# Optimization experiments

Measured on AMD Instinct MI355X. Metric: run time of the kernel, lower is better.

Reference implementation:

```python
import jax, jax.numpy as jnp
import numpy as np

N_NODES = 100000
N_EDGES = 1250000
NUM_RELS = 8
D_IN, D_HID, D_OUT = 64, 64, 32


def setup_inputs() -> dict:
    key = jax.random.key(0)
    ks = jax.random.split(key, 10)
    x = jax.random.normal(ks[0], (N_NODES, D_IN), dtype=jnp.float32)
    src = jax.random.randint(ks[1], (N_EDGES,), 0, N_NODES, dtype=jnp.int32)
    dst = jax.random.randint(ks[2], (N_EDGES,), 0, N_NODES, dtype=jnp.int32)
    edge_type = jax.random.randint(ks[3], (N_EDGES,), 0, NUM_RELS, dtype=jnp.int32)
    s1 = 1.0 / np.sqrt(D_IN)
    s2 = 1.0 / np.sqrt(D_HID)
    W1 = jax.random.uniform(ks[4], (NUM_RELS, D_IN, D_HID), jnp.float32, -s1, s1)
    root1 = jax.random.uniform(ks[5], (D_IN, D_HID), jnp.float32, -s1, s1)
    b1 = jnp.zeros((D_HID,), jnp.float32)
    W2 = jax.random.uniform(ks[6], (NUM_RELS, D_HID, D_OUT), jnp.float32, -s2, s2)
    root2 = jax.random.uniform(ks[7], (D_HID, D_OUT), jnp.float32, -s2, s2)
    b2 = jnp.zeros((D_OUT,), jnp.float32)
    return {"x": x, "W1": W1, "root1": root1, "b1": b1,
            "W2": W2, "root2": root2, "b2": b2,
            "src": src, "dst": dst, "edge_type": edge_type}


def rgcn_conv(x, W, root, b, src, dst, edge_type, num_rels, num_nodes):
    # self-loop (root) transform + bias
    out = x @ root + b
    for r in range(num_rels):  # loop over small fixed relation set
        mask = (edge_type == r).astype(x.dtype)          # (E,)
        h = x @ W[r]                                      # (N, dout): transform once per relation
        msg = h[src] * mask[:, None]                      # (E, dout) gather + mask
        agg = jax.ops.segment_sum(msg, dst, num_segments=num_nodes)
        cnt = jax.ops.segment_sum(mask, dst, num_segments=num_nodes)
        out = out + agg / jnp.maximum(cnt, 1.0)[:, None]  # per-relation mean (PyG default aggr)
    return out


def reference(x, W1, root1, b1, W2, root2, b2, src, dst, edge_type):
    h = jax.nn.relu(rgcn_conv(x, W1, root1, b1, src, dst, edge_type, NUM_RELS, N_NODES))
    return rgcn_conv(h, W2, root2, b2, src, dst, edge_type, NUM_RELS, N_NODES)
```

## Files before the change

kernel.cpp:

```cpp
#include <hip/hip_runtime.h>

typedef _Float16 half8 __attribute__((ext_vector_type(8)));
typedef __attribute__((ext_vector_type(4))) float f32x4;

__device__ __forceinline__ unsigned short f2h(float f) {
    _Float16 h = (_Float16)f;
    return *(unsigned short*)&h;
}
__device__ __forceinline__ float h2f(unsigned short u) {
    _Float16 h = *(_Float16*)&u;
    return (float)h;
}


__device__ __forceinline__ void wprep_body(
    const float* __restrict__ W, const float* __restrict__ root,
    unsigned short* __restrict__ wb, int dout, int idx)
{
    int c = idx / (64 * dout);
    int rme = idx % (64 * dout);
    int kk = rme / dout;
    int j = rme % dout;
    float f = (c == 0) ? root[kk * dout + j]
                       : W[(size_t)(c - 1) * 64 * dout + kk * dout + j];
    wb[(size_t)c * dout * 72 + (size_t)j * 72 + kk] = f2h(f);
}

__global__ __launch_bounds__(256) void prep_kernel(
    const float* __restrict__ x, unsigned short* __restrict__ xh, int n8,
    const float* __restrict__ W1, const float* __restrict__ root1,
    unsigned short* __restrict__ wb1,
    const float* __restrict__ W2, const float* __restrict__ root2,
    unsigned short* __restrict__ wb2,
    int* __restrict__ hist, int nhist4)
{
    int id = blockIdx.x * 256 + threadIdx.x;
    if (id < n8) {
        const f32x4* p = (const f32x4*)(x + (size_t)id * 8);
        f32x4 u = p[0], v = p[1];
        half8 o;
#pragma unroll
        for (int j = 0; j < 4; ++j) {
            o[j] = (_Float16)u[j];
            o[j + 4] = (_Float16)v[j];
        }
        *(half8*)(xh + (size_t)id * 8) = o;
        return;
    }
    id -= n8;
    if (id < 9 * 64 * 64) { wprep_body(W1, root1, wb1, 64, id); return; }
    id -= 9 * 64 * 64;
    if (id < 9 * 64 * 32) { wprep_body(W2, root2, wb2, 32, id); return; }
    id -= 9 * 64 * 32;
    if (id < nhist4) ((int4*)hist)[id] = make_int4(0, 0, 0, 0);
}


__global__ __launch_bounds__(256) void hist8_kernel(
    const int* __restrict__ dst, const int* __restrict__ et,
    int* __restrict__ hist, int E)
{
    int e = blockIdx.x * 256 + threadIdx.x;
    if (e < E) atomicAdd(&hist[dst[e] * 8 + et[e]], 1);
}

#define SCAN_TILE 4096
__global__ __launch_bounds__(1024) void scanA_kernel(
    const int* __restrict__ hist, int* __restrict__ bstart,
    int* __restrict__ partial, int nkeys)
{
    __shared__ int wsum[16];
    const int t = threadIdx.x;
    const int lane = t & 63, w = t >> 6;
    const int base = blockIdx.x * SCAN_TILE + t * 4;
    int v[4];
    int s = 0;
#pragma unroll
    for (int i = 0; i < 4; ++i) {
        v[i] = (base + i < nkeys) ? hist[base + i] : 0;
        s += v[i];
    }
    int inc = s;
#pragma unroll
    for (int off = 1; off < 64; off <<= 1) {
        int u = __shfl_up(inc, off);
        if (lane >= off) inc += u;
    }
    if (lane == 63) wsum[w] = inc;
    __syncthreads();
    if (w == 0 && lane < 16) {
        int ws = wsum[lane];
        int winc = ws;
#pragma unroll
        for (int off = 1; off < 16; off <<= 1) {
            int u = __shfl_up(winc, off);
            if (lane >= off) winc += u;
        }
        wsum[lane] = winc - ws;
    }
    __syncthreads();
    int run = wsum[w] + (inc - s);
#pragma unroll
    for (int i = 0; i < 4; ++i) {
        if (base + i < nkeys) bstart[base + i] = run;
        run += v[i];
    }
    if (t == 1023) partial[blockIdx.x] = run;
}

__global__ __launch_bounds__(64) void scanB_kernel(
    const int* __restrict__ partial, int* __restrict__ pscan,
    int* __restrict__ bstart_end, int nblk)
{
    const int lane = threadIdx.x;
    int running = 0;
    for (int b = 0; b < nblk; b += 64) {
        int i = b + lane;
        int o = (i < nblk) ? partial[i] : 0;
        int v = o;
#pragma unroll
        for (int off = 1; off < 64; off <<= 1) {
            int u = __shfl_up(v, off);
            if (lane >= off) v += u;
        }
        if (i < nblk) pscan[i] = running + v - o;
        running += __shfl(v, 63);
    }
    if (lane == 0) *bstart_end = running;
}

__global__ __launch_bounds__(256) void scatter_kernel(
    const int* __restrict__ src, const int* __restrict__ dst,
    const int* __restrict__ et, int* __restrict__ hist,
    const int* __restrict__ bstart, const int* __restrict__ pscan,
    unsigned* __restrict__ srt, int E)
{
    int e = blockIdx.x * 256 + threadIdx.x;
    if (e < E) {
        int key = dst[e] * 8 + et[e];
        int r = atomicSub(&hist[key], 1) - 1;
        srt[bstart[key] + pscan[key >> 12] + r] = (unsigned)src[e] << 6;
    }
}


template <int DOUT, int RELU, int OUTH>
__global__ __launch_bounds__(256, 6) void fused_kernel(
    const unsigned short* __restrict__ tab,
    const unsigned* __restrict__ srt,
    const int* __restrict__ bstart,
    const int* __restrict__ pscan,
    const unsigned short* __restrict__ wb,
    const float* __restrict__ bias,
    float* __restrict__ outf,
    unsigned short* __restrict__ outh,
    int n_nodes, int Etot)
{
    __shared__ __align__(16) unsigned short Atile[16 * 600];

    const int t = threadIdx.x;
    const int w = t >> 6, lane = t & 63;
    const int quad = lane >> 4, l16 = lane & 15;
    const int nbt = blockIdx.x * 16;
    const int nb4 = nbt + w * 4;
    const int KEYS = n_nodes * 8;

    {
        const int nb0 = nb4 * 8;
        int idx = nb0 + lane; if (idx > KEYS) idx = KEYS;
        int lv;
        if (idx < KEYS) lv = bstart[idx] + pscan[idx >> 12];
        else            lv = Etot;
        const int E0 = __builtin_amdgcn_readlane(lv, 0);
        const int E1 = __builtin_amdgcn_readlane(lv, 32);

        int cntv = __shfl_down(lv, 1) - lv;
        float rsc = 1.0f / fmaxf((float)cntv, 1.0f);

#pragma unroll
        for (int i = 0; i < 4; ++i) {
            int node = nb4 + i;
            unsigned short v = 0;
            if (node < n_nodes) v = tab[(size_t)node * 64 + lane];
            Atile[(w * 4 + i) * 600 + lane] = v;
        }

        float acc0 = 0.f, acc1 = 0.f;
        int R = 0;
        int bnext = __builtin_amdgcn_readlane(lv, 1);

        auto flushes = [&](int eabs) {
            while (R < 32 && eabs == bnext) {
                float sc = __uint_as_float(
                    __builtin_amdgcn_readlane(__float_as_uint(rsc), R));
                Atile[(w * 4 + (R >> 3)) * 600 + 64 + (R & 7) * 64 + lane] =
                    f2h((acc0 + acc1) * sc);
                acc0 = 0.f; acc1 = 0.f;
                ++R;
                bnext = (R < 31) ? __builtin_amdgcn_readlane(lv, R + 1) : E1;
            }
        };

        int base = E0;
        while (base < E1) {
            const int blen = min(64, E1 - base);
            unsigned rec = 0;
            if (lane < blen) rec = srt[base + lane];
            int k = 0;
            for (; k + 8 <= blen; k += 8) {
                unsigned q0 = __shfl(rec, k),     q1 = __shfl(rec, k + 1);
                unsigned q2 = __shfl(rec, k + 2), q3 = __shfl(rec, k + 3);
                unsigned q4 = __shfl(rec, k + 4), q5 = __shfl(rec, k + 5);
                unsigned q6 = __shfl(rec, k + 6), q7 = __shfl(rec, k + 7);
                float v0 = h2f(tab[q0 + lane]), v1 = h2f(tab[q1 + lane]);
                float v2 = h2f(tab[q2 + lane]), v3 = h2f(tab[q3 + lane]);
                float v4 = h2f(tab[q4 + lane]), v5 = h2f(tab[q5 + lane]);
                float v6 = h2f(tab[q6 + lane]), v7 = h2f(tab[q7 + lane]);
                flushes(base + k);     acc0 += v0;
                flushes(base + k + 1); acc1 += v1;
                flushes(base + k + 2); acc0 += v2;
                flushes(base + k + 3); acc1 += v3;
                flushes(base + k + 4); acc0 += v4;
                flushes(base + k + 5); acc1 += v5;
                flushes(base + k + 6); acc0 += v6;
                flushes(base + k + 7); acc1 += v7;
            }
            for (; k < blen; ++k) {
                unsigned q = __shfl(rec, k);
                float v = h2f(tab[q + lane]);
                flushes(base + k);
                acc0 += v;
            }
            base += 64;
        }
        flushes(E1);
        while (R < 32) {
            float sc = __uint_as_float(
                __builtin_amdgcn_readlane(__float_as_uint(rsc), R));
            Atile[(w * 4 + (R >> 3)) * 600 + 64 + (R & 7) * 64 + lane] =
                f2h((acc0 + acc1) * sc);
            acc0 = 0.f; acc1 = 0.f;
            ++R;
        }
    }

    __syncthreads();

    constexpr int JPW = DOUT / 16;
    if (JPW == 2 && w >= 2) return;

    const int j = w * 16 + l16;
    f32x4 d = {0.f, 0.f, 0.f, 0.f};
    const unsigned short* arow = &Atile[l16 * 600];
#pragma unroll
    for (int c = 0; c < 9; ++c) {
        half8 a0 = *(const half8*)(arow + c * 64 + quad * 8);
        half8 a1 = *(const half8*)(arow + c * 64 + 32 + quad * 8);
        half8 b0 = *(const half8*)&wb[c * DOUT * 72 + j * 72 + quad * 8];
        half8 b1 = *(const half8*)&wb[c * DOUT * 72 + j * 72 + 32 + quad * 8];
        d = __builtin_amdgcn_mfma_f32_16x16x32_f16(a0, b0, d, 0, 0, 0);
        d = __builtin_amdgcn_mfma_f32_16x16x32_f16(a1, b1, d, 0, 0, 0);
    }

    const float bj = bias[j];
#pragma unroll
    for (int r = 0; r < 4; ++r) {
        const int node = nbt + quad * 4 + r;
        if (node < n_nodes) {
            float v = d[r] + bj;
            if (RELU) v = fmaxf(v, 0.0f);
            if (OUTH) outh[(size_t)node * 64 + j] = f2h(v);
            else      outf[(size_t)node * DOUT + j] = v;
        }
    }
}

extern "C" void kernel_launch(void* const* d_in, const int* in_sizes, int n_in,
                              void* d_out, int out_size, void* d_ws, size_t ws_size,
                              hipStream_t stream) {
    const float* x     = (const float*)d_in[0];
    const float* W1    = (const float*)d_in[1];
    const float* root1 = (const float*)d_in[2];
    const float* b1    = (const float*)d_in[3];
    const float* W2    = (const float*)d_in[4];
    const float* root2 = (const float*)d_in[5];
    const float* b2    = (const float*)d_in[6];
    const int*   src   = (const int*)d_in[7];
    const int*   dst   = (const int*)d_in[8];
    const int*   et    = (const int*)d_in[9];

    const int N = in_sizes[0] / 64;
    const int E = in_sizes[7];
    const int KEYS = N * 8;

    char* p = (char*)d_ws;
    auto alloc = [&](size_t bytes) {
        char* r = p;
        p += (bytes + 15) & ~(size_t)15;
        return r;
    };
    unsigned* srt       = (unsigned*)alloc((size_t)E * 4);
    int* hist           = (int*)alloc((size_t)KEYS * 4);
    int* bstart         = (int*)alloc((size_t)(KEYS + 1) * 4);
    int* partial        = (int*)alloc(256 * 4);
    int* pscan          = (int*)alloc(256 * 4);
    unsigned short* wb1 = (unsigned short*)alloc((size_t)9 * 64 * 72 * 2);
    unsigned short* wb2 = (unsigned short*)alloc((size_t)9 * 32 * 72 * 2);
    unsigned short* xh  = (unsigned short*)alloc((size_t)N * 64 * 2);
    unsigned short* h   = (unsigned short*)alloc((size_t)N * 64 * 2);

    const int n8 = N * 8;
    const int nhist4 = KEYS / 4;
    const int prep_items = n8 + 9 * 64 * 64 + 9 * 64 * 32 + nhist4;
    prep_kernel<<<(prep_items + 255) / 256, 256, 0, stream>>>(
        x, xh, n8, W1, root1, wb1, W2, root2, wb2, hist, nhist4);

    hist8_kernel<<<(E + 255) / 256, 256, 0, stream>>>(dst, et, hist, E);
    const int nscan = (KEYS + SCAN_TILE - 1) / SCAN_TILE;
    scanA_kernel<<<nscan, 1024, 0, stream>>>(hist, bstart, partial, KEYS);
    scanB_kernel<<<1, 64, 0, stream>>>(partial, pscan, bstart + KEYS, nscan);
    scatter_kernel<<<(E + 255) / 256, 256, 0, stream>>>(
        src, dst, et, hist, bstart, pscan, srt, E);

    fused_kernel<64, 1, 1><<<(N + 15) / 16, 256, 0, stream>>>(
        xh, srt, bstart, pscan, wb1, b1, nullptr, h, N, E);
    fused_kernel<32, 0, 0><<<(N + 15) / 16, 256, 0, stream>>>(
        h, srt, bstart, pscan, wb2, b2, (float*)d_out, nullptr, N, E);
}
```

Before: 340.5 us.

## Accumulate per-relation neighbor sums in LDS with atomics instead of segment flushes

Edge records now pack the source index, the low bits of the destination node and the relation id. Each edge adds its gathered feature row into a per-wave shared-memory float accumulator (32 segments x 64 lanes) using LDS atomicAdd. This replaces the branchy segment-boundary flush logic and the shuffle broadcast of records. The cost is 32 KB of extra LDS per block, which is why launch bounds drop to 3 blocks per CU, plus LDS atomic traffic on every edge and scalar loads of srt per edge.

```diff
diff --git a/kernel.cpp b/kernel.cpp
--- a/kernel.cpp
+++ b/kernel.cpp
@@ -137,15 +137,17 @@
 {
     int e = blockIdx.x * 256 + threadIdx.x;
     if (e < E) {
-        int key = dst[e] * 8 + et[e];
-        int r = atomicSub(&hist[key], 1) - 1;
-        srt[bstart[key] + pscan[key >> 12] + r] = (unsigned)src[e] << 6;
+        int d = dst[e], r = et[e];
+        int key = d * 8 + r;
+        int c = atomicSub(&hist[key], 1) - 1;
+        srt[bstart[key] + pscan[key >> 12] + c] =
+            ((unsigned)src[e] << 5) | ((unsigned)(d & 3) << 3) | (unsigned)r;
     }
 }
 
 
 template <int DOUT, int RELU, int OUTH>
-__global__ __launch_bounds__(256, 6) void fused_kernel(
+__global__ __launch_bounds__(256, 3) void fused_kernel(
     const unsigned short* __restrict__ tab,
     const unsigned* __restrict__ srt,
     const int* __restrict__ bstart,
@@ -157,6 +159,7 @@
     int n_nodes, int Etot)
 {
     __shared__ __align__(16) unsigned short Atile[16 * 600];
+    __shared__ __align__(16) float FAcc[4][32 * 64];
 
     const int t = threadIdx.x;
     const int w = t >> 6, lane = t & 63;
@@ -178,6 +181,9 @@
         float rsc = 1.0f / fmaxf((float)cntv, 1.0f);
 
 #pragma unroll
+        for (int i = 0; i < 32; ++i) FAcc[w][i * 64 + lane] = 0.f;
+
+#pragma unroll
         for (int i = 0; i < 4; ++i) {
             int node = nb4 + i;
             unsigned short v = 0;
@@ -185,62 +191,27 @@
             Atile[(w * 4 + i) * 600 + lane] = v;
         }
 
-        float acc0 = 0.f, acc1 = 0.f;
-        int R = 0;
-        int bnext = __builtin_amdgcn_readlane(lv, 1);
-
-        auto flushes = [&](int eabs) {
-            while (R < 32 && eabs == bnext) {
-                float sc = __uint_as_float(
-                    __builtin_amdgcn_readlane(__float_as_uint(rsc), R));
-                Atile[(w * 4 + (R >> 3)) * 600 + 64 + (R & 7) * 64 + lane] =
-                    f2h((acc0 + acc1) * sc);
-                acc0 = 0.f; acc1 = 0.f;
-                ++R;
-                bnext = (R < 31) ? __builtin_amdgcn_readlane(lv, R + 1) : E1;
+        int e = E0;
+        for (; e + 8 <= E1; e += 8) {
+#pragma unroll
+            for (int i = 0; i < 8; ++i) {
+                unsigned rq = srt[e + i];
+                float v = h2f(tab[(size_t)(rq >> 5) * 64 + lane]);
+                atomicAdd(&FAcc[w][(rq & 31u) * 64 + lane], v);
             }
-        };
-
-        int base = E0;
-        while (base < E1) {
-            const int blen = min(64, E1 - base);
-            unsigned rec = 0;
-            if (lane < blen) rec = srt[base + lane];
-            int k = 0;
-            for (; k + 8 <= blen; k += 8) {
-                unsigned q0 = __shfl(rec, k),     q1 = __shfl(rec, k + 1);
-                unsigned q2 = __shfl(rec, k + 2), q3 = __shfl(rec, k + 3);
-                unsigned q4 = __shfl(rec, k + 4), q5 = __shfl(rec, k + 5);
-                unsigned q6 = __shfl(rec, k + 6), q7 = __shfl(rec, k + 7);
-                float v0 = h2f(tab[q0 + lane]), v1 = h2f(tab[q1 + lane]);
-                float v2 = h2f(tab[q2 + lane]), v3 = h2f(tab[q3 + lane]);
-                float v4 = h2f(tab[q4 + lane]), v5 = h2f(tab[q5 + lane]);
-                float v6 = h2f(tab[q6 + lane]), v7 = h2f(tab[q7 + lane]);
-                flushes(base + k);     acc0 += v0;
-                flushes(base + k + 1); acc1 += v1;
-                flushes(base + k + 2); acc0 += v2;
-                flushes(base + k + 3); acc1 += v3;
-                flushes(base + k + 4); acc0 += v4;
-                flushes(base + k + 5); acc1 += v5;
-                flushes(base + k + 6); acc0 += v6;
-                flushes(base + k + 7); acc1 += v7;
-            }
-            for (; k < blen; ++k) {
-                unsigned q = __shfl(rec, k);
-                float v = h2f(tab[q + lane]);
-                flushes(base + k);
-                acc0 += v;
-            }
-            base += 64;
-        }
-        flushes(E1);
-        while (R < 32) {
+        }
+        for (; e < E1; ++e) {
+            unsigned rq = srt[e];
+            float v = h2f(tab[(size_t)(rq >> 5) * 64 + lane]);
+            atomicAdd(&FAcc[w][(rq & 31u) * 64 + lane], v);
+        }
+
+#pragma unroll
+        for (int R = 0; R < 32; ++R) {
             float sc = __uint_as_float(
                 __builtin_amdgcn_readlane(__float_as_uint(rsc), R));
             Atile[(w * 4 + (R >> 3)) * 600 + 64 + (R & 7) * 64 + lane] =
-                f2h((acc0 + acc1) * sc);
-            acc0 = 0.f; acc1 = 0.f;
-            ++R;
+                f2h(FAcc[w][R * 64 + lane] * sc);
         }
     }
 
```

Result: slower. 1.083 ms (+217.9%).
